# Optimization experiments

Measured on AMD Instinct MI355X. Metric: run time of the kernel, lower is better.

Reference implementation:

```python
import jax, jax.numpy as jnp
import numpy as np

N_NODES = 100000
N_EDGES = 1600000
IN_DIM = 64
EMB_DIM = 64
NUM_EDGE_EMB = 4
BN_EPS = 1e-5


def setup_inputs() -> dict:
    key = jax.random.key(0)
    ks = jax.random.split(key, 10)
    x = jax.random.normal(ks[0], (N_NODES, IN_DIM), dtype=jnp.float32)
    edge_index = jax.random.randint(ks[1], (2, N_EDGES), 0, N_NODES, dtype=jnp.int32)
    edge_attr = jax.random.randint(ks[2], (N_EDGES,), 0, NUM_EDGE_EMB, dtype=jnp.int32)
    # learned params
    edge_emb_table = jax.random.normal(ks[3], (NUM_EDGE_EMB, IN_DIM), dtype=jnp.float32)
    s1 = 1.0 / np.sqrt(IN_DIM)
    W1 = jax.random.uniform(ks[4], (IN_DIM, EMB_DIM), jnp.float32, -s1, s1)
    b1 = jax.random.uniform(ks[5], (EMB_DIM,), jnp.float32, -s1, s1)
    gamma = jnp.ones((EMB_DIM,), jnp.float32)
    beta = jnp.zeros((EMB_DIM,), jnp.float32)
    s2 = 1.0 / np.sqrt(EMB_DIM)
    W2 = jax.random.uniform(ks[6], (EMB_DIM, EMB_DIM), jnp.float32, -s2, s2)
    b2 = jax.random.uniform(ks[7], (EMB_DIM,), jnp.float32, -s2, s2)
    eps = jnp.zeros((), jnp.float32)  # train_eps=True, initial value 0
    return {
        "x": x,
        "edge_emb_table": edge_emb_table,
        "eps": eps,
        "W1": W1,
        "b1": b1,
        "gamma": gamma,
        "beta": beta,
        "W2": W2,
        "b2": b2,
        "edge_index": edge_index,
        "edge_attr": edge_attr,
    }


def reference(x, edge_emb_table, eps, W1, b1, gamma, beta, W2, b2, edge_index, edge_attr):
    src, dst = edge_index[0], edge_index[1]
    # GINEConv message: relu(x_j + e_ij), gathered over edges  [E, in_dim]
    msg = jax.nn.relu(x[src] + edge_emb_table[edge_attr])
    # scatter-sum aggregation to target nodes  [N, in_dim]
    agg = jax.ops.segment_sum(msg, dst, num_segments=N_NODES)
    h = (1.0 + eps) * x + agg
    # MLP: Linear -> BatchNorm1d (batch stats) -> ReLU -> Linear
    h = h @ W1 + b1
    mu = jnp.mean(h, axis=0)
    var = jnp.var(h, axis=0)  # biased, as torch BN uses for normalization
    h = (h - mu) * jax.lax.rsqrt(var + BN_EPS) * gamma + beta
    h = jax.nn.relu(h)
    return h @ W2 + b2
```

## Files before the change

kernel.cpp:

```cpp
#include <hip/hip_runtime.h>

#define N_NODESC 100000
#define N_EDGESC 1600000
#define BN_EPSC 1e-5f
#define NBUCK 1024
#define NUSED 782
#define SBLK 256
#define EPB (N_EDGESC / SBLK)
#define MT 128
#define BCAP 4608
#define BCAPG 2304

__global__ __launch_bounds__(1024) void k_castsort(
    const int* __restrict__ ei, const int* __restrict__ ea,
    const float* __restrict__ x, uint2* __restrict__ xh4,
    int* __restrict__ gcur, int* __restrict__ tmp)
{
    __shared__ int ledge[EPB + 22];
    __shared__ int cnt[NBUCK];
    __shared__ int cstart[NBUCK + 1];
    __shared__ int cur[NBUCK];
    __shared__ int gofs[NBUCK];
    __shared__ int wtot[16];
    const int t = threadIdx.x;
    const int k = blockIdx.x;

    cnt[t] = 0;
    {
        const float4* x4 = (const float4*)x;
        const int g = k * 1024 + t;
        float4 v[7];
        bool m[7];
        #pragma unroll
        for (int i = 0; i < 7; i++) {
            const int idx = g + i * (SBLK * 1024);
            m[i] = (idx < N_NODESC * 16);
            if (m[i]) v[i] = x4[idx];
        }
        #pragma unroll
        for (int i = 0; i < 7; i++) {
            if (m[i]) {
                const int idx = g + i * (SBLK * 1024);
                unsigned int a = __float_as_uint(v[i].x);
                unsigned int b = __float_as_uint(v[i].y);
                unsigned int c = __float_as_uint(v[i].z);
                unsigned int d = __float_as_uint(v[i].w);
                a = (a + 0x7FFFu + ((a >> 16) & 1u)) >> 16;
                b = (b + 0x7FFFu + ((b >> 16) & 1u)) >> 16;
                c = (c + 0x7FFFu + ((c >> 16) & 1u)) >> 16;
                d = (d + 0x7FFFu + ((d >> 16) & 1u)) >> 16;
                xh4[idx] = make_uint2(a | (b << 16), c | (d << 16));
            }
        }
    }
    __syncthreads();

    int pk[7], bk[7];
    const int base = k * EPB;
    #pragma unroll
    for (int i = 0; i < 7; i++) {
        const int e = base + i * 1024 + t;
        if (e < base + EPB) {
            const int src = ei[e];
            const int dst = ei[N_EDGESC + e];
            const int a = ea[e];
            pk[i] = src | (a << 17) | ((dst & 127) << 19);
            bk[i] = dst >> 7;
            atomicAdd(&cnt[bk[i]], 1);
        } else bk[i] = -1;
    }
    __syncthreads();

    {
        const int lane = t & 63;
        const int w = t >> 6;
        const int v = cnt[t];
        int inc = v;
        #pragma unroll
        for (int d = 1; d < 64; d <<= 1) {
            const int u = __shfl_up(inc, d);
            if (lane >= d) inc += u;
        }
        if (lane == 63) wtot[w] = inc;
        __syncthreads();
        int add = 0;
        #pragma unroll
        for (int w2 = 0; w2 < 16; w2++) if (w2 < w) add += wtot[w2];
        const int ex = inc - v + add;
        cstart[t] = ex;
        cur[t] = ex;
        if (t == 1023) cstart[NBUCK] = ex + v;
    }
    __syncthreads();

    #pragma unroll
    for (int i = 0; i < 7; i++) {
        if (bk[i] >= 0) {
            const int pos = atomicAdd(&cur[bk[i]], 1);
            ledge[pos] = pk[i];
        }
    }
    {
        const int c = cnt[t];
        if (c > 0) gofs[t] = atomicAdd(&gcur[t], c);
    }
    __syncthreads();

    for (int i = t; i < EPB; i += 1024) {
        int lo = 0, hi = NBUCK;
        #pragma unroll
        for (int s = 0; s < 10; s++) {
            const int mid = (lo + hi) >> 1;
            if (cstart[mid] <= i) lo = mid; else hi = mid;
        }
        const int o = gofs[lo] + (i - cstart[lo]);
        if (o < BCAPG) tmp[lo * BCAPG + o] = ledge[i];
    }
}

__global__ __launch_bounds__(512) void k_aggf(
    const ushort* __restrict__ xh, const float* __restrict__ emb,
    const float* __restrict__ x, const float* __restrict__ epsp,
    const int* __restrict__ gcur, const int* __restrict__ tmp,
    float* __restrict__ agg)
{
    __shared__ int packedL[BCAP];
    __shared__ int cnt[128];
    __shared__ int cst[128];
    __shared__ int cur[128];
    __shared__ float emL[4][68];
    const int t = threadIdx.x;
    const int b = blockIdx.x;
    const int start = b * BCAPG;
    int cntb = gcur[b];
    if (cntb > BCAPG) cntb = BCAPG;
    if (t < 128) cnt[t] = 0;
    if (t < 256) emL[t >> 6][t & 63] = emb[t];
    __syncthreads();

    for (int e = t; e < cntb; e += 512)
        atomicAdd(&cnt[(tmp[start + e] >> 19) & 127], 1);
    __syncthreads();
    if (t < 64) {
        const int lane = t;
        const int v0 = cnt[lane];
        const int v1 = cnt[64 + lane];
        int i0 = v0, i1 = v1;
        #pragma unroll
        for (int d = 1; d < 64; d <<= 1) {
            const int u0 = __shfl_up(i0, d);
            const int u1 = __shfl_up(i1, d);
            if (lane >= d) { i0 += u0; i1 += u1; }
        }
        const int tot0 = __shfl(i0, 63);
        cst[lane] = i0 - v0;
        cst[64 + lane] = tot0 + i1 - v1;
        cur[lane] = i0 - v0;
        cur[64 + lane] = tot0 + i1 - v1;
    }
    __syncthreads();
    for (int e = t; e < cntb; e += 512) {
        const int p = tmp[start + e];
        const int pos = atomicAdd(&cur[(p >> 19) & 127], 1);
        if (pos < BCAP) packedL[pos] = p;
    }
    __syncthreads();

    const int g = t >> 3;
    const int q = t & 7;
    const float sc1 = 1.0f + epsp[0];
    const uint4* xv8 = (const uint4*)xh;
    const float4* x4 = (const float4*)x;
    float4* o4 = (float4*)agg;
    const float* eq = &emL[0][0] + q * 8;
    for (int j = 0; j < 2; j++) {
        const int nl = g * 2 + j;
        const int n = b * 128 + nl;
        int e = cst[nl];
        const int ee = cur[nl];
        float4 aL = make_float4(0.f, 0.f, 0.f, 0.f);
        float4 aH = make_float4(0.f, 0.f, 0.f, 0.f);
        if (n < N_NODESC) {
            const float4 v0 = x4[(size_t)n * 16 + q * 2];
            const float4 v1 = x4[(size_t)n * 16 + q * 2 + 1];
            aL.x = sc1 * v0.x; aL.y = sc1 * v0.y;
            aL.z = sc1 * v0.z; aL.w = sc1 * v0.w;
            aH.x = sc1 * v1.x; aH.y = sc1 * v1.y;
            aH.z = sc1 * v1.z; aH.w = sc1 * v1.w;
        }
        for (; e + 2 <= ee; e += 2) {
            const int p0 = packedL[e];
            const int p1 = packedL[e + 1];
            const uint4 u0 = xv8[(size_t)(p0 & 0x1FFFF) * 8 + q];
            const uint4 u1 = xv8[(size_t)(p1 & 0x1FFFF) * 8 + q];
            const float* e0 = eq + ((p0 >> 17) & 3) * 68;
            const float* e1 = eq + ((p1 >> 17) & 3) * 68;
            const float4 t0L = *(const float4*)(e0);
            const float4 t0H = *(const float4*)(e0 + 4);
            const float4 t1L = *(const float4*)(e1);
            const float4 t1H = *(const float4*)(e1 + 4);
            aL.x += fmaxf(__uint_as_float(u0.x << 16)          + t0L.x, 0.f)
                  + fmaxf(__uint_as_float(u1.x << 16)          + t1L.x, 0.f);
            aL.y += fmaxf(__uint_as_float(u0.x & 0xFFFF0000u)  + t0L.y, 0.f)
                  + fmaxf(__uint_as_float(u1.x & 0xFFFF0000u)  + t1L.y, 0.f);
            aL.z += fmaxf(__uint_as_float(u0.y << 16)          + t0L.z, 0.f)
                  + fmaxf(__uint_as_float(u1.y << 16)          + t1L.z, 0.f);
            aL.w += fmaxf(__uint_as_float(u0.y & 0xFFFF0000u)  + t0L.w, 0.f)
                  + fmaxf(__uint_as_float(u1.y & 0xFFFF0000u)  + t1L.w, 0.f);
            aH.x += fmaxf(__uint_as_float(u0.z << 16)          + t0H.x, 0.f)
                  + fmaxf(__uint_as_float(u1.z << 16)          + t1H.x, 0.f);
            aH.y += fmaxf(__uint_as_float(u0.z & 0xFFFF0000u)  + t0H.y, 0.f)
                  + fmaxf(__uint_as_float(u1.z & 0xFFFF0000u)  + t1H.y, 0.f);
            aH.z += fmaxf(__uint_as_float(u0.w << 16)          + t0H.z, 0.f)
                  + fmaxf(__uint_as_float(u1.w << 16)          + t1H.z, 0.f);
            aH.w += fmaxf(__uint_as_float(u0.w & 0xFFFF0000u)  + t0H.w, 0.f)
                  + fmaxf(__uint_as_float(u1.w & 0xFFFF0000u)  + t1H.w, 0.f);
        }
        for (; e < ee; e++) {
            const int p0 = packedL[e];
            const uint4 u0 = xv8[(size_t)(p0 & 0x1FFFF) * 8 + q];
            const float* e0 = eq + ((p0 >> 17) & 3) * 68;
            const float4 t0L = *(const float4*)(e0);
            const float4 t0H = *(const float4*)(e0 + 4);
            aL.x += fmaxf(__uint_as_float(u0.x << 16)         + t0L.x, 0.f);
            aL.y += fmaxf(__uint_as_float(u0.x & 0xFFFF0000u) + t0L.y, 0.f);
            aL.z += fmaxf(__uint_as_float(u0.y << 16)         + t0L.z, 0.f);
            aL.w += fmaxf(__uint_as_float(u0.y & 0xFFFF0000u) + t0L.w, 0.f);
            aH.x += fmaxf(__uint_as_float(u0.z << 16)         + t0H.x, 0.f);
            aH.y += fmaxf(__uint_as_float(u0.z & 0xFFFF0000u) + t0H.y, 0.f);
            aH.z += fmaxf(__uint_as_float(u0.w << 16)         + t0H.z, 0.f);
            aH.w += fmaxf(__uint_as_float(u0.w & 0xFFFF0000u) + t0H.w, 0.f);
        }
        if (n < N_NODESC) {
            o4[(size_t)n * 16 + q * 2]     = aL;
            o4[(size_t)n * 16 + q * 2 + 1] = aH;
        }
    }
}

__global__ __launch_bounds__(256) void k_mlp1(
    float* hbuf,
    const float* __restrict__ W1, const float* __restrict__ b1,
    float* __restrict__ cs, float* __restrict__ css)
{
    __shared__ float lin[MT][68];
    __shared__ float lW[4096];
    __shared__ float redS[4][64];
    __shared__ float redQ[4][64];
    const int t = threadIdx.x;
    const int nbase = blockIdx.x * MT;

    {
        const float4* W4 = (const float4*)W1;
        float4* lW4 = (float4*)lW;
        #pragma unroll
        for (int i = 0; i < 4; i++) lW4[i * 256 + t] = W4[i * 256 + t];
    }
    {
        const float4* a4 = (const float4*)hbuf;
        #pragma unroll
        for (int i = 0; i < 8; i++) {
            const int fidx = i * 256 + t;
            const int row = fidx >> 4;
            const int q = fidx & 15;
            const int n = nbase + row;
            float4 v = make_float4(0.f, 0.f, 0.f, 0.f);
            if (n < N_NODESC) v = a4[(size_t)n * 16 + q];
            *(float4*)&lin[row][q * 4] = v;
        }
    }
    __syncthreads();

    const int g = t & 7;
    const int r0 = t >> 3;
    const float4* lW4 = (const float4*)lW;
    const float4* b4 = (const float4*)b1;
    const float4 bb0 = b4[g * 2 + 0];
    const float4 bb1 = b4[g * 2 + 1];
    float4 a00 = bb0, a01 = bb1, a10 = bb0, a11 = bb1;
    float4 a20 = bb0, a21 = bb1, a30 = bb0, a31 = bb1;
    for (int k = 0; k < 64; k++) {
        const float v0 = lin[r0][k];
        const float v1 = lin[r0 + 32][k];
        const float v2 = lin[r0 + 64][k];
        const float v3 = lin[r0 + 96][k];
        const float4 w0 = lW4[k * 16 + g * 2 + 0];
        const float4 w1 = lW4[k * 16 + g * 2 + 1];
        a00.x = fmaf(v0, w0.x, a00.x); a00.y = fmaf(v0, w0.y, a00.y);
        a00.z = fmaf(v0, w0.z, a00.z); a00.w = fmaf(v0, w0.w, a00.w);
        a01.x = fmaf(v0, w1.x, a01.x); a01.y = fmaf(v0, w1.y, a01.y);
        a01.z = fmaf(v0, w1.z, a01.z); a01.w = fmaf(v0, w1.w, a01.w);
        a10.x = fmaf(v1, w0.x, a10.x); a10.y = fmaf(v1, w0.y, a10.y);
        a10.z = fmaf(v1, w0.z, a10.z); a10.w = fmaf(v1, w0.w, a10.w);
        a11.x = fmaf(v1, w1.x, a11.x); a11.y = fmaf(v1, w1.y, a11.y);
        a11.z = fmaf(v1, w1.z, a11.z); a11.w = fmaf(v1, w1.w, a11.w);
        a20.x = fmaf(v2, w0.x, a20.x); a20.y = fmaf(v2, w0.y, a20.y);
        a20.z = fmaf(v2, w0.z, a20.z); a20.w = fmaf(v2, w0.w, a20.w);
        a21.x = fmaf(v2, w1.x, a21.x); a21.y = fmaf(v2, w1.y, a21.y);
        a21.z = fmaf(v2, w1.z, a21.z); a21.w = fmaf(v2, w1.w, a21.w);
        a30.x = fmaf(v3, w0.x, a30.x); a30.y = fmaf(v3, w0.y, a30.y);
        a30.z = fmaf(v3, w0.z, a30.z); a30.w = fmaf(v3, w0.w, a30.w);
        a31.x = fmaf(v3, w1.x, a31.x); a31.y = fmaf(v3, w1.y, a31.y);
        a31.z = fmaf(v3, w1.z, a31.z); a31.w = fmaf(v3, w1.w, a31.w);
    }

    float4 A0[4] = {a00, a10, a20, a30};
    float4 A1[4] = {a01, a11, a21, a31};
    float4* h4 = (float4*)hbuf;
    float msk[4];
    #pragma unroll
    for (int j = 0; j < 4; j++) {
        const int n = nbase + r0 + 32 * j;
        msk[j] = (n < N_NODESC) ? 1.0f : 0.0f;
        if (n < N_NODESC) {
            h4[(size_t)n * 16 + g * 2 + 0] = A0[j];
            h4[(size_t)n * 16 + g * 2 + 1] = A1[j];
        }
    }

    float vs[8], vq[8];
    #pragma unroll
    for (int c = 0; c < 8; c++) { vs[c] = 0.f; vq[c] = 0.f; }
    #pragma unroll
    for (int j = 0; j < 4; j++) {
        const float e0[8] = {A0[j].x, A0[j].y, A0[j].z, A0[j].w,
                             A1[j].x, A1[j].y, A1[j].z, A1[j].w};
        #pragma unroll
        for (int c = 0; c < 8; c++) {
            const float v = e0[c] * msk[j];
            vs[c] += v;
            vq[c] += v * e0[c];
        }
    }
    #pragma unroll
    for (int o = 8; o < 64; o <<= 1) {
        #pragma unroll
        for (int c = 0; c < 8; c++) {
            vs[c] += __shfl_xor(vs[c], o);
            vq[c] += __shfl_xor(vq[c], o);
        }
    }
    const int lane = t & 63;
    const int w = t >> 6;
    if (lane < 8) {
        #pragma unroll
        for (int c = 0; c < 8; c++) {
            redS[w][lane * 8 + c] = vs[c];
            redQ[w][lane * 8 + c] = vq[c];
        }
    }
    __syncthreads();
    if (t < 64) {
        const float s = redS[0][t] + redS[1][t] + redS[2][t] + redS[3][t];
        const float qq = redQ[0][t] + redQ[1][t] + redQ[2][t] + redQ[3][t];
        unsafeAtomicAdd(&cs[t], s);
        unsafeAtomicAdd(&css[t], qq);
    }
}

__global__ __launch_bounds__(256) void k_mlp2(
    const float* h1, const float* __restrict__ W2, const float* __restrict__ b2,
    const float* __restrict__ gamma, const float* __restrict__ beta,
    const float* __restrict__ cs, const float* __restrict__ css,
    float* out)
{
    __shared__ float lin[MT][68];
    __shared__ float lW[4096];
    __shared__ float scl[64];
    __shared__ float sft[64];
    const int t = threadIdx.x;
    const int nbase = blockIdx.x * MT;

    if (t < 64) {
        const float inv = 1.0f / (float)N_NODESC;
        const float mu = cs[t] * inv;
        const float var = css[t] * inv - mu * mu;
        const float rs = rsqrtf(var + BN_EPSC);
        const float s = rs * gamma[t];
        scl[t] = s;
        sft[t] = fmaf(-mu, s, beta[t]);
    }
    {
        const float4* W4 = (const float4*)W2;
        float4* lW4 = (float4*)lW;
        #pragma unroll
        for (int i = 0; i < 4; i++) lW4[i * 256 + t] = W4[i * 256 + t];
    }
    __syncthreads();
    {
        const float4* h4 = (const float4*)h1;
        #pragma unroll
        for (int i = 0; i < 8; i++) {
            const int fidx = i * 256 + t;
            const int row = fidx >> 4;
            const int q = fidx & 15;
            const int n = nbase + row;
            float4 v = make_float4(0.f, 0.f, 0.f, 0.f);
            if (n < N_NODESC) {
                const float4 h = h4[(size_t)n * 16 + q];
                const int c = q * 4;
                v.x = fmaxf(fmaf(h.x, scl[c + 0], sft[c + 0]), 0.f);
                v.y = fmaxf(fmaf(h.y, scl[c + 1], sft[c + 1]), 0.f);
                v.z = fmaxf(fmaf(h.z, scl[c + 2], sft[c + 2]), 0.f);
                v.w = fmaxf(fmaf(h.w, scl[c + 3], sft[c + 3]), 0.f);
            }
            *(float4*)&lin[row][q * 4] = v;
        }
    }
    __syncthreads();

    const int g = t & 7;
    const int r0 = t >> 3;
    const float4* lW4 = (const float4*)lW;
    const float4* b4 = (const float4*)b2;
    const float4 bb0 = b4[g * 2 + 0];
    const float4 bb1 = b4[g * 2 + 1];
    float4 a00 = bb0, a01 = bb1, a10 = bb0, a11 = bb1;
    float4 a20 = bb0, a21 = bb1, a30 = bb0, a31 = bb1;
    for (int k = 0; k < 64; k++) {
        const float v0 = lin[r0][k];
        const float v1 = lin[r0 + 32][k];
        const float v2 = lin[r0 + 64][k];
        const float v3 = lin[r0 + 96][k];
        const float4 w0 = lW4[k * 16 + g * 2 + 0];
        const float4 w1 = lW4[k * 16 + g * 2 + 1];
        a00.x = fmaf(v0, w0.x, a00.x); a00.y = fmaf(v0, w0.y, a00.y);
        a00.z = fmaf(v0, w0.z, a00.z); a00.w = fmaf(v0, w0.w, a00.w);
        a01.x = fmaf(v0, w1.x, a01.x); a01.y = fmaf(v0, w1.y, a01.y);
        a01.z = fmaf(v0, w1.z, a01.z); a01.w = fmaf(v0, w1.w, a01.w);
        a10.x = fmaf(v1, w0.x, a10.x); a10.y = fmaf(v1, w0.y, a10.y);
        a10.z = fmaf(v1, w0.z, a10.z); a10.w = fmaf(v1, w0.w, a10.w);
        a11.x = fmaf(v1, w1.x, a11.x); a11.y = fmaf(v1, w1.y, a11.y);
        a11.z = fmaf(v1, w1.z, a11.z); a11.w = fmaf(v1, w1.w, a11.w);
        a20.x = fmaf(v2, w0.x, a20.x); a20.y = fmaf(v2, w0.y, a20.y);
        a20.z = fmaf(v2, w0.z, a20.z); a20.w = fmaf(v2, w0.w, a20.w);
        a21.x = fmaf(v2, w1.x, a21.x); a21.y = fmaf(v2, w1.y, a21.y);
        a21.z = fmaf(v2, w1.z, a21.z); a21.w = fmaf(v2, w1.w, a21.w);
        a30.x = fmaf(v3, w0.x, a30.x); a30.y = fmaf(v3, w0.y, a30.y);
        a30.z = fmaf(v3, w0.z, a30.z); a30.w = fmaf(v3, w0.w, a30.w);
        a31.x = fmaf(v3, w1.x, a31.x); a31.y = fmaf(v3, w1.y, a31.y);
        a31.z = fmaf(v3, w1.z, a31.z); a31.w = fmaf(v3, w1.w, a31.w);
    }
    const float4 A0[4] = {a00, a10, a20, a30};
    const float4 A1[4] = {a01, a11, a21, a31};
    float4* o4 = (float4*)out;
    #pragma unroll
    for (int j = 0; j < 4; j++) {
        const int n = nbase + r0 + 32 * j;
        if (n < N_NODESC) {
            o4[(size_t)n * 16 + g * 2 + 0] = A0[j];
            o4[(size_t)n * 16 + g * 2 + 1] = A1[j];
        }
    }
}

extern "C" void kernel_launch(void* const* d_in, const int* in_sizes, int n_in,
                              void* d_out, int out_size, void* d_ws, size_t ws_size,
                              hipStream_t stream) {
    const float* x     = (const float*)d_in[0];
    const float* emb   = (const float*)d_in[1];
    const float* eps   = (const float*)d_in[2];
    const float* W1    = (const float*)d_in[3];
    const float* b1    = (const float*)d_in[4];
    const float* gamma = (const float*)d_in[5];
    const float* beta  = (const float*)d_in[6];
    const float* W2    = (const float*)d_in[7];
    const float* b2    = (const float*)d_in[8];
    const int*   ei    = (const int*)d_in[9];
    const int*   ea    = (const int*)d_in[10];
    float* out = (float*)d_out;

    float* ws    = (float*)d_ws;
    float* cs    = ws;
    float* css   = ws + 64;
    int*   gcur  = (int*)(ws + 128);
    int*   tmp   = gcur + NBUCK;
    ushort* xh   = (ushort*)(tmp + (size_t)NBUCK * BCAPG);

    hipMemsetAsync(d_ws, 0, (size_t)(128 + NBUCK) * sizeof(int), stream);

    k_castsort<<<SBLK, 1024, 0, stream>>>(ei, ea, x, (uint2*)xh, gcur, tmp);
    k_aggf<<<NUSED, 512, 0, stream>>>(xh, emb, x, eps, gcur, tmp, out);
    k_mlp1<<<NUSED, 256, 0, stream>>>(out, W1, b1, cs, css);
    k_mlp2<<<NUSED, 256, 0, stream>>>(out, W2, b2, gamma, beta, cs, css, out);
}
```

Baseline: 213.4 us.

## Fuse aggregation kernel with first MLP linear layer and BN stats

Merges the edge aggregation kernel and the first linear plus batch-statistics kernel into one. The aggregated rows now stay in shared memory and feed the W1 matmul directly, so the intermediate agg array no longer makes a global round trip and one launch is dropped. The matmul is re-tiled for 512 threads with two rows per thread, and the reduction scratch reuses the packedL shared buffer. Shared memory per block grows to roughly 70KB, which may lower occupancy of the gather-heavy aggregation phase.

Measured after the change: 202.7 us. -5.0%, faster.

```diff
diff --git a/kernel.cpp b/kernel.cpp
--- a/kernel.cpp
+++ b/kernel.cpp
@@ -118,13 +118,16 @@
     }
 }
 
-__global__ __launch_bounds__(512) void k_aggf(
+__global__ __launch_bounds__(512) void k_aggmlp1(
     const ushort* __restrict__ xh, const float* __restrict__ emb,
     const float* __restrict__ x, const float* __restrict__ epsp,
     const int* __restrict__ gcur, const int* __restrict__ tmp,
-    float* __restrict__ agg)
+    const float* __restrict__ W1, const float* __restrict__ b1,
+    float* __restrict__ out, float* __restrict__ cs, float* __restrict__ css)
 {
     __shared__ int packedL[BCAP];
+    __shared__ float lin[MT][68];
+    __shared__ float lW[4096];
     __shared__ int cnt[128];
     __shared__ int cst[128];
     __shared__ int cur[128];
@@ -132,6 +135,13 @@
     const int t = threadIdx.x;
     const int b = blockIdx.x;
     const int start = b * BCAPG;
+
+    {
+        const float4* W4 = (const float4*)W1;
+        float4* lW4s = (float4*)lW;
+        lW4s[t] = W4[t];
+        lW4s[512 + t] = W4[512 + t];
+    }
     int cntb = gcur[b];
     if (cntb > BCAPG) cntb = BCAPG;
     if (t < 128) cnt[t] = 0;
@@ -166,126 +176,90 @@
     }
     __syncthreads();
 
-    const int g = t >> 3;
-    const int q = t & 7;
-    const float sc1 = 1.0f + epsp[0];
-    const uint4* xv8 = (const uint4*)xh;
-    const float4* x4 = (const float4*)x;
-    float4* o4 = (float4*)agg;
-    const float* eq = &emL[0][0] + q * 8;
-    for (int j = 0; j < 2; j++) {
-        const int nl = g * 2 + j;
-        const int n = b * 128 + nl;
-        int e = cst[nl];
-        const int ee = cur[nl];
-        float4 aL = make_float4(0.f, 0.f, 0.f, 0.f);
-        float4 aH = make_float4(0.f, 0.f, 0.f, 0.f);
-        if (n < N_NODESC) {
-            const float4 v0 = x4[(size_t)n * 16 + q * 2];
-            const float4 v1 = x4[(size_t)n * 16 + q * 2 + 1];
-            aL.x = sc1 * v0.x; aL.y = sc1 * v0.y;
-            aL.z = sc1 * v0.z; aL.w = sc1 * v0.w;
-            aH.x = sc1 * v1.x; aH.y = sc1 * v1.y;
-            aH.z = sc1 * v1.z; aH.w = sc1 * v1.w;
-        }
-        for (; e + 2 <= ee; e += 2) {
-            const int p0 = packedL[e];
-            const int p1 = packedL[e + 1];
-            const uint4 u0 = xv8[(size_t)(p0 & 0x1FFFF) * 8 + q];
-            const uint4 u1 = xv8[(size_t)(p1 & 0x1FFFF) * 8 + q];
-            const float* e0 = eq + ((p0 >> 17) & 3) * 68;
-            const float* e1 = eq + ((p1 >> 17) & 3) * 68;
-            const float4 t0L = *(const float4*)(e0);
-            const float4 t0H = *(const float4*)(e0 + 4);
-            const float4 t1L = *(const float4*)(e1);
-            const float4 t1H = *(const float4*)(e1 + 4);
-            aL.x += fmaxf(__uint_as_float(u0.x << 16)          + t0L.x, 0.f)
-                  + fmaxf(__uint_as_float(u1.x << 16)          + t1L.x, 0.f);
-            aL.y += fmaxf(__uint_as_float(u0.x & 0xFFFF0000u)  + t0L.y, 0.f)
-                  + fmaxf(__uint_as_float(u1.x & 0xFFFF0000u)  + t1L.y, 0.f);
-            aL.z += fmaxf(__uint_as_float(u0.y << 16)          + t0L.z, 0.f)
-                  + fmaxf(__uint_as_float(u1.y << 16)          + t1L.z, 0.f);
-            aL.w += fmaxf(__uint_as_float(u0.y & 0xFFFF0000u)  + t0L.w, 0.f)
-                  + fmaxf(__uint_as_float(u1.y & 0xFFFF0000u)  + t1L.w, 0.f);
-            aH.x += fmaxf(__uint_as_float(u0.z << 16)          + t0H.x, 0.f)
-                  + fmaxf(__uint_as_float(u1.z << 16)          + t1H.x, 0.f);
-            aH.y += fmaxf(__uint_as_float(u0.z & 0xFFFF0000u)  + t0H.y, 0.f)
-                  + fmaxf(__uint_as_float(u1.z & 0xFFFF0000u)  + t1H.y, 0.f);
-            aH.z += fmaxf(__uint_as_float(u0.w << 16)          + t0H.z, 0.f)
-                  + fmaxf(__uint_as_float(u1.w << 16)          + t1H.z, 0.f);
-            aH.w += fmaxf(__uint_as_float(u0.w & 0xFFFF0000u)  + t0H.w, 0.f)
-                  + fmaxf(__uint_as_float(u1.w & 0xFFFF0000u)  + t1H.w, 0.f);
-        }
-        for (; e < ee; e++) {
-            const int p0 = packedL[e];
-            const uint4 u0 = xv8[(size_t)(p0 & 0x1FFFF) * 8 + q];
-            const float* e0 = eq + ((p0 >> 17) & 3) * 68;
-            const float4 t0L = *(const float4*)(e0);
-            const float4 t0H = *(const float4*)(e0 + 4);
-            aL.x += fmaxf(__uint_as_float(u0.x << 16)         + t0L.x, 0.f);
-            aL.y += fmaxf(__uint_as_float(u0.x & 0xFFFF0000u) + t0L.y, 0.f);
-            aL.z += fmaxf(__uint_as_float(u0.y << 16)         + t0L.z, 0.f);
-            aL.w += fmaxf(__uint_as_float(u0.y & 0xFFFF0000u) + t0L.w, 0.f);
-            aH.x += fmaxf(__uint_as_float(u0.z << 16)         + t0H.x, 0.f);
-            aH.y += fmaxf(__uint_as_float(u0.z & 0xFFFF0000u) + t0H.y, 0.f);
-            aH.z += fmaxf(__uint_as_float(u0.w << 16)         + t0H.z, 0.f);
-            aH.w += fmaxf(__uint_as_float(u0.w & 0xFFFF0000u) + t0H.w, 0.f);
-        }
-        if (n < N_NODESC) {
-            o4[(size_t)n * 16 + q * 2]     = aL;
-            o4[(size_t)n * 16 + q * 2 + 1] = aH;
-        }
-    }
-}
-
-__global__ __launch_bounds__(256) void k_mlp1(
-    float* hbuf,
-    const float* __restrict__ W1, const float* __restrict__ b1,
-    float* __restrict__ cs, float* __restrict__ css)
-{
-    __shared__ float lin[MT][68];
-    __shared__ float lW[4096];
-    __shared__ float redS[4][64];
-    __shared__ float redQ[4][64];
-    const int t = threadIdx.x;
-    const int nbase = blockIdx.x * MT;
-
-    {
-        const float4* W4 = (const float4*)W1;
-        float4* lW4 = (float4*)lW;
-        #pragma unroll
-        for (int i = 0; i < 4; i++) lW4[i * 256 + t] = W4[i * 256 + t];
-    }
-    {
-        const float4* a4 = (const float4*)hbuf;
-        #pragma unroll
-        for (int i = 0; i < 8; i++) {
-            const int fidx = i * 256 + t;
-            const int row = fidx >> 4;
-            const int q = fidx & 15;
-            const int n = nbase + row;
-            float4 v = make_float4(0.f, 0.f, 0.f, 0.f);
-            if (n < N_NODESC) v = a4[(size_t)n * 16 + q];
-            *(float4*)&lin[row][q * 4] = v;
-        }
-    }
-    __syncthreads();
-
-    const int g = t & 7;
+    {
+        const int g = t >> 3;
+        const int q = t & 7;
+        const float sc1 = 1.0f + epsp[0];
+        const uint4* xv8 = (const uint4*)xh;
+        const float4* x4 = (const float4*)x;
+        const float* eq = &emL[0][0] + q * 8;
+        for (int j = 0; j < 2; j++) {
+            const int nl = g * 2 + j;
+            const int n = b * 128 + nl;
+            int e = cst[nl];
+            const int ee = cur[nl];
+            float4 aL = make_float4(0.f, 0.f, 0.f, 0.f);
+            float4 aH = make_float4(0.f, 0.f, 0.f, 0.f);
+            if (n < N_NODESC) {
+                const float4 v0 = x4[(size_t)n * 16 + q * 2];
+                const float4 v1 = x4[(size_t)n * 16 + q * 2 + 1];
+                aL.x = sc1 * v0.x; aL.y = sc1 * v0.y;
+                aL.z = sc1 * v0.z; aL.w = sc1 * v0.w;
+                aH.x = sc1 * v1.x; aH.y = sc1 * v1.y;
+                aH.z = sc1 * v1.z; aH.w = sc1 * v1.w;
+            }
+            for (; e + 2 <= ee; e += 2) {
+                const int p0 = packedL[e];
+                const int p1 = packedL[e + 1];
+                const uint4 u0 = xv8[(size_t)(p0 & 0x1FFFF) * 8 + q];
+                const uint4 u1 = xv8[(size_t)(p1 & 0x1FFFF) * 8 + q];
+                const float* e0 = eq + ((p0 >> 17) & 3) * 68;
+                const float* e1 = eq + ((p1 >> 17) & 3) * 68;
+                const float4 t0L = *(const float4*)(e0);
+                const float4 t0H = *(const float4*)(e0 + 4);
+                const float4 t1L = *(const float4*)(e1);
+                const float4 t1H = *(const float4*)(e1 + 4);
+                aL.x += fmaxf(__uint_as_float(u0.x << 16)          + t0L.x, 0.f)
+                      + fmaxf(__uint_as_float(u1.x << 16)          + t1L.x, 0.f);
+                aL.y += fmaxf(__uint_as_float(u0.x & 0xFFFF0000u)  + t0L.y, 0.f)
+                      + fmaxf(__uint_as_float(u1.x & 0xFFFF0000u)  + t1L.y, 0.f);
+                aL.z += fmaxf(__uint_as_float(u0.y << 16)          + t0L.z, 0.f)
+                      + fmaxf(__uint_as_float(u1.y << 16)          + t1L.z, 0.f);
+                aL.w += fmaxf(__uint_as_float(u0.y & 0xFFFF0000u)  + t0L.w, 0.f)
+                      + fmaxf(__uint_as_float(u1.y & 0xFFFF0000u)  + t1L.w, 0.f);
+                aH.x += fmaxf(__uint_as_float(u0.z << 16)          + t0H.x, 0.f)
+                      + fmaxf(__uint_as_float(u1.z << 16)          + t1H.x, 0.f);
+                aH.y += fmaxf(__uint_as_float(u0.z & 0xFFFF0000u)  + t0H.y, 0.f)
+                      + fmaxf(__uint_as_float(u1.z & 0xFFFF0000u)  + t1H.y, 0.f);
+                aH.z += fmaxf(__uint_as_float(u0.w << 16)          + t0H.z, 0.f)
+                      + fmaxf(__uint_as_float(u1.w << 16)          + t1H.z, 0.f);
+                aH.w += fmaxf(__uint_as_float(u0.w & 0xFFFF0000u)  + t0H.w, 0.f)
+                      + fmaxf(__uint_as_float(u1.w & 0xFFFF0000u)  + t1H.w, 0.f);
+            }
+            for (; e < ee; e++) {
+                const int p0 = packedL[e];
+                const uint4 u0 = xv8[(size_t)(p0 & 0x1FFFF) * 8 + q];
+                const float* e0 = eq + ((p0 >> 17) & 3) * 68;
+                const float4 t0L = *(const float4*)(e0);
+                const float4 t0H = *(const float4*)(e0 + 4);
+                aL.x += fmaxf(__uint_as_float(u0.x << 16)         + t0L.x, 0.f);
+                aL.y += fmaxf(__uint_as_float(u0.x & 0xFFFF0000u) + t0L.y, 0.f);
+                aL.z += fmaxf(__uint_as_float(u0.y << 16)         + t0L.z, 0.f);
+                aL.w += fmaxf(__uint_as_float(u0.y & 0xFFFF0000u) + t0L.w, 0.f);
+                aH.x += fmaxf(__uint_as_float(u0.z << 16)         + t0H.x, 0.f);
+                aH.y += fmaxf(__uint_as_float(u0.z & 0xFFFF0000u) + t0H.y, 0.f);
+                aH.z += fmaxf(__uint_as_float(u0.w << 16)         + t0H.z, 0.f);
+                aH.w += fmaxf(__uint_as_float(u0.w & 0xFFFF0000u) + t0H.w, 0.f);
+            }
+            *(float4*)&lin[nl][q * 8]     = aL;
+            *(float4*)&lin[nl][q * 8 + 4] = aH;
+        }
+    }
+    __syncthreads();
+
+    const int gc = t & 7;
     const int r0 = t >> 3;
     const float4* lW4 = (const float4*)lW;
     const float4* b4 = (const float4*)b1;
-    const float4 bb0 = b4[g * 2 + 0];
-    const float4 bb1 = b4[g * 2 + 1];
-    float4 a00 = bb0, a01 = bb1, a10 = bb0, a11 = bb1;
-    float4 a20 = bb0, a21 = bb1, a30 = bb0, a31 = bb1;
+    const float4 bb0 = b4[gc * 2 + 0];
+    const float4 bb1 = b4[gc * 2 + 1];
+    float4 a00 = bb0, a01 = bb1;
+    float4 a10 = bb0, a11 = bb1;
     for (int k = 0; k < 64; k++) {
         const float v0 = lin[r0][k];
-        const float v1 = lin[r0 + 32][k];
-        const float v2 = lin[r0 + 64][k];
-        const float v3 = lin[r0 + 96][k];
-        const float4 w0 = lW4[k * 16 + g * 2 + 0];
-        const float4 w1 = lW4[k * 16 + g * 2 + 1];
+        const float v1 = lin[r0 + 64][k];
+        const float4 w0 = lW4[k * 16 + gc * 2 + 0];
+        const float4 w1 = lW4[k * 16 + gc * 2 + 1];
         a00.x = fmaf(v0, w0.x, a00.x); a00.y = fmaf(v0, w0.y, a00.y);
         a00.z = fmaf(v0, w0.z, a00.z); a00.w = fmaf(v0, w0.w, a00.w);
         a01.x = fmaf(v0, w1.x, a01.x); a01.y = fmaf(v0, w1.y, a01.y);
@@ -294,42 +268,33 @@
         a10.z = fmaf(v1, w0.z, a10.z); a10.w = fmaf(v1, w0.w, a10.w);
         a11.x = fmaf(v1, w1.x, a11.x); a11.y = fmaf(v1, w1.y, a11.y);
         a11.z = fmaf(v1, w1.z, a11.z); a11.w = fmaf(v1, w1.w, a11.w);
-        a20.x = fmaf(v2, w0.x, a20.x); a20.y = fmaf(v2, w0.y, a20.y);
-        a20.z = fmaf(v2, w0.z, a20.z); a20.w = fmaf(v2, w0.w, a20.w);
-        a21.x = fmaf(v2, w1.x, a21.x); a21.y = fmaf(v2, w1.y, a21.y);
-        a21.z = fmaf(v2, w1.z, a21.z); a21.w = fmaf(v2, w1.w, a21.w);
-        a30.x = fmaf(v3, w0.x, a30.x); a30.y = fmaf(v3, w0.y, a30.y);
-        a30.z = fmaf(v3, w0.z, a30.z); a30.w = fmaf(v3, w0.w, a30.w);
-        a31.x = fmaf(v3, w1.x, a31.x); a31.y = fmaf(v3, w1.y, a31.y);
-        a31.z = fmaf(v3, w1.z, a31.z); a31.w = fmaf(v3, w1.w, a31.w);
-    }
-
-    float4 A0[4] = {a00, a10, a20, a30};
-    float4 A1[4] = {a01, a11, a21, a31};
-    float4* h4 = (float4*)hbuf;
-    float msk[4];
-    #pragma unroll
-    for (int j = 0; j < 4; j++) {
-        const int n = nbase + r0 + 32 * j;
-        msk[j] = (n < N_NODESC) ? 1.0f : 0.0f;
-        if (n < N_NODESC) {
-            h4[(size_t)n * 16 + g * 2 + 0] = A0[j];
-            h4[(size_t)n * 16 + g * 2 + 1] = A1[j];
-        }
+    }
+    const int n0 = b * MT + r0;
+    const int n1 = n0 + 64;
+    const float msk0 = (n0 < N_NODESC) ? 1.0f : 0.0f;
+    const float msk1 = (n1 < N_NODESC) ? 1.0f : 0.0f;
+    float4* o4 = (float4*)out;
+    if (n0 < N_NODESC) {
+        o4[(size_t)n0 * 16 + gc * 2 + 0] = a00;
+        o4[(size_t)n0 * 16 + gc * 2 + 1] = a01;
+    }
+    if (n1 < N_NODESC) {
+        o4[(size_t)n1 * 16 + gc * 2 + 0] = a10;
+        o4[(size_t)n1 * 16 + gc * 2 + 1] = a11;
     }
 
     float vs[8], vq[8];
-    #pragma unroll
-    for (int c = 0; c < 8; c++) { vs[c] = 0.f; vq[c] = 0.f; }
-    #pragma unroll
-    for (int j = 0; j < 4; j++) {
-        const float e0[8] = {A0[j].x, A0[j].y, A0[j].z, A0[j].w,
-                             A1[j].x, A1[j].y, A1[j].z, A1[j].w};
+    {
+        const float e0[8] = {a00.x, a00.y, a00.z, a00.w,
+                             a01.x, a01.y, a01.z, a01.w};
+        const float e1[8] = {a10.x, a10.y, a10.z, a10.w,
+                             a11.x, a11.y, a11.z, a11.w};
         #pragma unroll
         for (int c = 0; c < 8; c++) {
-            const float v = e0[c] * msk[j];
-            vs[c] += v;
-            vq[c] += v * e0[c];
+            const float v0 = e0[c] * msk0;
+            const float v1 = e1[c] * msk1;
+            vs[c] = v0 + v1;
+            vq[c] = v0 * e0[c] + v1 * e1[c];
         }
     }
     #pragma unroll
@@ -340,19 +305,26 @@
             vq[c] += __shfl_xor(vq[c], o);
         }
     }
+    __syncthreads();
+    float* redS = (float*)packedL;
+    float* redQ = redS + 512;
     const int lane = t & 63;
     const int w = t >> 6;
     if (lane < 8) {
         #pragma unroll
         for (int c = 0; c < 8; c++) {
-            redS[w][lane * 8 + c] = vs[c];
-            redQ[w][lane * 8 + c] = vq[c];
+            redS[w * 64 + lane * 8 + c] = vs[c];
+            redQ[w * 64 + lane * 8 + c] = vq[c];
         }
     }
     __syncthreads();
     if (t < 64) {
-        const float s = redS[0][t] + redS[1][t] + redS[2][t] + redS[3][t];
-        const float qq = redQ[0][t] + redQ[1][t] + redQ[2][t] + redQ[3][t];
+        float s = 0.f, qq = 0.f;
+        #pragma unroll
+        for (int w2 = 0; w2 < 8; w2++) {
+            s  += redS[w2 * 64 + t];
+            qq += redQ[w2 * 64 + t];
+        }
         unsafeAtomicAdd(&cs[t], s);
         unsafeAtomicAdd(&css[t], qq);
     }
@@ -480,7 +452,7 @@
     hipMemsetAsync(d_ws, 0, (size_t)(128 + NBUCK) * sizeof(int), stream);
 
     k_castsort<<<SBLK, 1024, 0, stream>>>(ei, ea, x, (uint2*)xh, gcur, tmp);
-    k_aggf<<<NUSED, 512, 0, stream>>>(xh, emb, x, eps, gcur, tmp, out);
-    k_mlp1<<<NUSED, 256, 0, stream>>>(out, W1, b1, cs, css);
+    k_aggmlp1<<<NUSED, 512, 0, stream>>>(xh, emb, x, eps, gcur, tmp,
+                                         W1, b1, out, cs, css);
     k_mlp2<<<NUSED, 256, 0, stream>>>(out, W2, b2, gamma, beta, cs, css, out);
 }
```
